# Kernel tuning notes

Measured on AMD Instinct MI355X. Metric: run time of the kernel, lower is better.

The kernel has to match this reference:

```python
import jax, jax.numpy as jnp
import numpy as np

N_TOK = 16384   # total tokens (batch*seq)
H = 2048        # hidden_size
I = 768         # moe_intermediate_size (per-expert MLP width)
TOPK = 8        # num_experts_per_tok


def setup_inputs() -> dict:
    key = jax.random.key(0)
    ks = jax.random.split(key, 7)
    hidden_states = jax.random.normal(ks[0], (N_TOK, H), dtype=jnp.float32)
    # expert_mask[j, k] != 0 means token k selected this expert at top-k slot j
    expert_mask = jax.random.randint(ks[1], (TOPK, N_TOK), 0, 2, dtype=jnp.int32)
    routing_weights = jax.random.uniform(ks[2], (N_TOK, TOPK), dtype=jnp.float32)
    final_hidden_states = jax.random.normal(ks[3], (N_TOK, H), dtype=jnp.float32)
    gate_w = jax.random.normal(ks[4], (I, H), dtype=jnp.float32) * 0.02
    up_w = jax.random.normal(ks[5], (I, H), dtype=jnp.float32) * 0.02
    down_w = jax.random.normal(ks[6], (H, I), dtype=jnp.float32) * 0.02
    return {
        "hidden_states": hidden_states,
        "expert_mask": expert_mask,
        "routing_weights": routing_weights,
        "final_hidden_states": final_hidden_states,
        "gate_w": gate_w,
        "up_w": up_w,
        "down_w": down_w,
    }


def reference(hidden_states, expert_mask, routing_weights, final_hidden_states,
              gate_w, up_w, down_w):
    # forward_expert: gather selected tokens, SwiGLU MLP, scale by routing weight,
    # scatter-add into final_hidden_states. Equivalent jit-friendly form: the
    # combined routing weight per token is w[k] = sum_j mask[j,k]*routing_weights[k,j]
    # (tokens selected multiple times are summed, matching index_add_ semantics),
    # and unselected tokens get w[k]=0 so they contribute nothing.
    g = hidden_states @ gate_w.T                       # [N, I]
    u = hidden_states @ up_w.T                         # [N, I]
    y = (jax.nn.silu(g) * u) @ down_w.T                # [N, H]
    w = jnp.einsum('jk,kj->k', expert_mask.astype(y.dtype), routing_weights)  # [N]
    return final_hidden_states + y * w[:, None]
```

## Files before the change

### kernel.cpp

```cpp
#include <hip/hip_runtime.h>
#include <stdint.h>

#define NTOK 16384
#define HD   2048
#define ID   768
#define TOPK 8

typedef __bf16 bf16x8 __attribute__((ext_vector_type(8)));
typedef float  floatx4 __attribute__((ext_vector_type(4)));
typedef unsigned short ushort8 __attribute__((ext_vector_type(8)));

__device__ __forceinline__ unsigned short f32_to_bf16_rne(float f) {
    union { float f; uint32_t u; } v; v.f = f;
    uint32_t u = v.u;
    u += 0x7FFFu + ((u >> 16) & 1u);
    return (unsigned short)(u >> 16);
}
__device__ __forceinline__ float bf16_to_f32(unsigned short h) {
    union { uint32_t u; float f; } v; v.u = ((uint32_t)h) << 16;
    return v.f;
}

#define GLD_LDS(gsrc, ldst)                                                              \
    __builtin_amdgcn_global_load_lds(                                                    \
        (const __attribute__((address_space(1))) uint32_t*)(const void*)(gsrc),          \
        (__attribute__((address_space(3))) uint32_t*)(void*)(ldst), 16, 0, 0)

template<int VM> __device__ __forceinline__ void wait_vm() {
    if constexpr (VM == 8)      asm volatile("s_waitcnt vmcnt(8)" ::: "memory");
    else if constexpr (VM == 4) asm volatile("s_waitcnt vmcnt(4)" ::: "memory");
    else if constexpr (VM == 3) asm volatile("s_waitcnt vmcnt(3)" ::: "memory");
    else                        asm volatile("s_waitcnt vmcnt(0)" ::: "memory");
}
#define BARRIER() do { asm volatile("" ::: "memory");              \
                       __builtin_amdgcn_s_barrier();               \
                       asm volatile("" ::: "memory"); } while (0)

__global__ __launch_bounds__(256) void compute_w_kernel(const int* __restrict__ mask,
                                                        const float* __restrict__ rw,
                                                        float* __restrict__ w) {
    int k = blockIdx.x * 256 + threadIdx.x;
    if (k >= NTOK) return;
    float acc = 0.f;
#pragma unroll
    for (int j = 0; j < TOPK; ++j)
        acc += (float)mask[j * NTOK + k] * rw[k * TOPK + j];
    w[k] = acc;
}

__global__ __launch_bounds__(256) void convert_hs_kernel(const float* __restrict__ src,
                                                         unsigned short* __restrict__ dst) {
    size_t i = (size_t)blockIdx.x * 256 + threadIdx.x;
    const float4* s = (const float4*)src;
    float4 a = s[2 * i], b = s[2 * i + 1];
    ushort8 o;
    o[0] = f32_to_bf16_rne(a.x); o[1] = f32_to_bf16_rne(a.y);
    o[2] = f32_to_bf16_rne(a.z); o[3] = f32_to_bf16_rne(a.w);
    o[4] = f32_to_bf16_rne(b.x); o[5] = f32_to_bf16_rne(b.y);
    o[6] = f32_to_bf16_rne(b.z); o[7] = f32_to_bf16_rne(b.w);
    *(ushort8*)(dst + 8 * i) = o;
}

__global__ __launch_bounds__(256) void convert_w3_kernel(const float* __restrict__ g,
                                                         const float* __restrict__ u,
                                                         const float* __restrict__ d,
                                                         unsigned short* __restrict__ dst) {
    int i = blockIdx.x * 256 + threadIdx.x;
    size_t e = (size_t)i * 8;
    const float* src;
    if (e < (size_t)2 * ID * HD) {
        int rd = (int)(e / HD);
        int c  = (int)(e - (size_t)rd * HD);
        int b = rd >> 4, h = (rd >> 3) & 1, sub = rd & 7;
        src = (h ? u : g) + (size_t)(b * 8 + sub) * HD + c;
    } else {
        src = d + (e - (size_t)2 * ID * HD);
    }
    const float4* s = (const float4*)src;
    float4 a = s[0], bq = s[1];
    ushort8 o;
    o[0] = f32_to_bf16_rne(a.x);  o[1] = f32_to_bf16_rne(a.y);
    o[2] = f32_to_bf16_rne(a.z);  o[3] = f32_to_bf16_rne(a.w);
    o[4] = f32_to_bf16_rne(bq.x); o[5] = f32_to_bf16_rne(bq.y);
    o[6] = f32_to_bf16_rne(bq.z); o[7] = f32_to_bf16_rne(bq.w);
    *(ushort8*)(dst + e) = o;
}

__global__ __launch_bounds__(512, 1) void gemm_gu_kernel(
    const unsigned short* __restrict__ A,
    const unsigned short* __restrict__ B,
    unsigned short* __restrict__ act) {
    constexpr int K = HD;
    constexpr int NT = K / 64;
    __shared__ __align__(16) unsigned char lds[2][57344];

    const int bid = blockIdx.x, nwg = gridDim.x;
    const int nb = (bid & 7) * (nwg >> 3) + (bid >> 3);
    const int bx = nb & 7, by = nb >> 3;
    const int row0 = by * 256, col0 = bx * 192;

    const int tid = threadIdx.x, wid = tid >> 6, lane = tid & 63;
    const int wr = wid >> 2, wc = wid & 3;
    const int lrow = lane & 15, q = lane >> 4;
    const int rsw = ((q ^ ((lrow >> 1) & 3)) << 4);

    const int kswz = (((lane & 3) ^ ((lane >> 3) & 3)) << 3);
    const unsigned short* sA[2];
#pragma unroll
    for (int h = 0; h < 2; ++h) {
        const int o = h * 8192 + wid * 1024 + lane * 16;
        sA[h] = A + (size_t)(row0 + (o >> 6)) * K + kswz;
    }
    const unsigned short* sB[3];
#pragma unroll
    for (int r = 0; r < 3; ++r) {
        const int o = r * 8192 + tid * 16;
        const int ks = (o >= 12288) ? 1 : 0;
        const int brow = (o - ks * 12288) >> 6;
        sB[r] = B + (size_t)(col0 + brow) * K + ks * 32 + kswz;
    }

#define STAGE_A(sb, ks, kt) do {                                                            \
        GLD_LDS(sA[0] + (kt) * 64 + (ks) * 32, lds[sb] + (ks) * 16384 + wid * 1024);        \
        GLD_LDS(sA[1] + (kt) * 64 + (ks) * 32, lds[sb] + (ks) * 16384 + 8192 + wid * 1024); \
    } while (0)
#define STAGE_B01(sb, kt) do {                                                              \
        GLD_LDS(sB[0] + (kt) * 64, lds[sb] + 32768 + wid * 1024);                           \
        GLD_LDS(sB[1] + (kt) * 64, lds[sb] + 32768 + 8192 + wid * 1024);                    \
    } while (0)
#define STAGE_B2(sb, kt)                                                                    \
        GLD_LDS(sB[2] + (kt) * 64, lds[sb] + 32768 + 16384 + wid * 1024)

#define READ_A(s, ks) do { const unsigned char* rgn = lds[s] + (ks) * 16384;                \
        _Pragma("unroll")                                                                   \
        for (int m = 0; m < 8; ++m)                                                         \
            af[m] = *(const bf16x8*)(rgn + (wr * 128 + m * 16 + lrow) * 64 + rsw);          \
    } while (0)
#define READ_B(s, ks) do { const unsigned char* rgn = lds[s] + 32768 + (ks) * 12288;        \
        _Pragma("unroll")                                                                   \
        for (int n = 0; n < 3; ++n)                                                         \
            bb[n] = *(const bf16x8*)(rgn + (wc * 48 + n * 16 + lrow) * 64 + rsw);           \
    } while (0)
#define MFMA_H(mh) do {                                                                     \
        __builtin_amdgcn_s_setprio(1);                                                      \
        _Pragma("unroll")                                                                   \
        for (int m = (mh) * 4; m < (mh) * 4 + 4; ++m)                                       \
            _Pragma("unroll")                                                               \
            for (int n = 0; n < 3; ++n)                                                     \
                acc[m][n] = __builtin_amdgcn_mfma_f32_16x16x32_bf16(af[m], bb[n], acc[m][n], 0, 0, 0); \
        __builtin_amdgcn_s_setprio(0);                                                      \
    } while (0)

    floatx4 acc[8][3];
#pragma unroll
    for (int m = 0; m < 8; ++m)
#pragma unroll
        for (int n = 0; n < 3; ++n) acc[m][n] = (floatx4){0.f, 0.f, 0.f, 0.f};
    bf16x8 af[8], bb[3];

    STAGE_A(0, 0, 0);
    STAGE_B01(0, 0);
    STAGE_A(0, 1, 0);
    STAGE_B2(0, 0);
    wait_vm<3>();
    BARRIER();

    for (int t = 0; t < NT - 1; ++t) {
        const int s = t & 1, sn = s ^ 1;
        READ_A(s, 0); READ_B(s, 0);
        STAGE_A(sn, 0, t + 1);
        MFMA_H(0);
        BARRIER();
        STAGE_B01(sn, t + 1);
        MFMA_H(1);
        wait_vm<4>();
        BARRIER();
        READ_A(s, 1); READ_B(s, 1);
        STAGE_A(sn, 1, t + 1);
        MFMA_H(0);
        BARRIER();
        STAGE_B2(sn, t + 1);
        MFMA_H(1);
        wait_vm<3>();
        BARRIER();
    }
    {
        const int s = (NT - 1) & 1;
        READ_A(s, 0); READ_B(s, 0);
        MFMA_H(0);
        BARRIER();
        MFMA_H(1);
        wait_vm<0>();
        BARRIER();
        READ_A(s, 1); READ_B(s, 1);
        MFMA_H(0);
        MFMA_H(1);
    }
#undef STAGE_A
#undef STAGE_B01
#undef STAGE_B2
#undef READ_A
#undef READ_B
#undef MFMA_H

#pragma unroll
    for (int m = 0; m < 8; ++m) {
        const int rowb = row0 + wr * 128 + m * 16 + q * 4;
        float sv[3][4];
#pragma unroll
        for (int n = 0; n < 3; ++n)
#pragma unroll
            for (int r = 0; r < 4; ++r) {
                const float gf = acc[m][n][r];
                const float uf = __shfl_xor(gf, 8, 64);
                const float sig = __builtin_amdgcn_rcpf(1.f + __expf(-gf));
                sv[n][r] = gf * sig * uf;
            }
        if ((lrow & 8) == 0) {
            const int ib0 = (col0 >> 1) + wc * 24 + lrow;
#pragma unroll
            for (int n = 0; n < 3; ++n)
#pragma unroll
                for (int r = 0; r < 4; ++r)
                    act[(size_t)(rowb + r) * ID + ib0 + n * 8] = f32_to_bf16_rne(sv[n][r]);
        }
    }
}

__global__ __launch_bounds__(256, 2) void gemm_down_kernel(
    const unsigned short* __restrict__ A,
    const unsigned short* __restrict__ B,
    const float* __restrict__ fin,
    const float* __restrict__ wtok,
    float* __restrict__ out) {
    constexpr int K = ID;
    constexpr int NT = K / 64;
    __shared__ __align__(16) unsigned char lds[2][32768];

    const int bid = blockIdx.x, nwg = gridDim.x;
    const int nb = (bid & 7) * (nwg >> 3) + (bid >> 3);
    const int bx = nb & 15, by = nb >> 4;
    const int row0 = by * 128, col0 = bx * 128;

    const int tid = threadIdx.x, wid = tid >> 6, lane = tid & 63;
    const int wr = wid >> 1, wc = wid & 1;
    const int lrow = lane & 15, q = lane >> 4;

    const int srow = wid * 8 + (lane >> 3);
    const int sk = (((lane & 7) ^ ((lane >> 3) & 7)) << 3);
    const unsigned short* sA[4];
    const unsigned short* sB[4];
#pragma unroll
    for (int r = 0; r < 4; ++r) {
        sA[r] = A + (size_t)(row0 + r * 32 + srow) * K + sk;
        sB[r] = B + (size_t)(col0 + r * 32 + srow) * K + sk;
    }

#define STAGE_T(sb, kt) do {                                                    \
        _Pragma("unroll")                                                       \
        for (int r = 0; r < 4; ++r)                                             \
            GLD_LDS(sA[r] + (kt) * 64, lds[sb] + r * 4096 + wid * 1024);        \
        _Pragma("unroll")                                                       \
        for (int r = 0; r < 4; ++r)                                             \
            GLD_LDS(sB[r] + (kt) * 64, lds[sb] + 16384 + r * 4096 + wid * 1024);\
    } while (0)

    floatx4 acc[4][4];
#pragma unroll
    for (int m = 0; m < 4; ++m)
#pragma unroll
        for (int n = 0; n < 4; ++n) acc[m][n] = (floatx4){0.f, 0.f, 0.f, 0.f};
    bf16x8 af[4], bb[4];

    STAGE_T(0, 0);

    for (int t = 0; t < NT; ++t) {
        const int s = t & 1;
        if (t + 1 < NT) {
            STAGE_T(s ^ 1, t + 1);
            wait_vm<8>();
        } else {
            wait_vm<0>();
        }
        BARRIER();
        const unsigned char* la = lds[s];
        const unsigned char* lb = lds[s] + 16384;
#pragma unroll
        for (int ks = 0; ks < 2; ++ks) {
#pragma unroll
            for (int m = 0; m < 4; ++m)
                af[m] = *(const bf16x8*)(la + (wr * 64 + m * 16 + lrow) * 128 +
                                         (((ks * 4 + q) ^ (lrow & 7)) << 4));
#pragma unroll
            for (int n = 0; n < 4; ++n)
                bb[n] = *(const bf16x8*)(lb + (wc * 64 + n * 16 + lrow) * 128 +
                                         (((ks * 4 + q) ^ (lrow & 7)) << 4));
            __builtin_amdgcn_s_setprio(1);
#pragma unroll
            for (int m = 0; m < 4; ++m)
#pragma unroll
                for (int n = 0; n < 4; ++n)
                    acc[m][n] = __builtin_amdgcn_mfma_f32_16x16x32_bf16(af[m], bb[n], acc[m][n], 0, 0, 0);
            __builtin_amdgcn_s_setprio(0);
        }
        BARRIER();
    }
#undef STAGE_T

#pragma unroll
    for (int m = 0; m < 4; ++m)
#pragma unroll
        for (int r = 0; r < 4; ++r) {
            const int row = row0 + wr * 64 + m * 16 + q * 4 + r;
            const float wv = wtok[row];
#pragma unroll
            for (int n = 0; n < 4; ++n) {
                const int col = col0 + wc * 64 + n * 16 + lrow;
                out[(size_t)row * HD + col] = fin[(size_t)row * HD + col] + wv * acc[m][n][r];
            }
        }
}

extern "C" void kernel_launch(void* const* d_in, const int* in_sizes, int n_in,
                              void* d_out, int out_size, void* d_ws, size_t ws_size,
                              hipStream_t stream) {
    const float* hs   = (const float*)d_in[0];
    const int*   mask = (const int*)d_in[1];
    const float* rw   = (const float*)d_in[2];
    const float* fin  = (const float*)d_in[3];
    const float* gw   = (const float*)d_in[4];
    const float* uw   = (const float*)d_in[5];
    const float* dw   = (const float*)d_in[6];
    float* out = (float*)d_out;

    char* ws = (char*)d_ws;
    unsigned short* hs_b   = (unsigned short*)ws; ws += (size_t)NTOK * HD * 2;
    unsigned short* wcat_b = (unsigned short*)ws; ws += (size_t)3 * ID * HD * 2;
    unsigned short* act_b  = (unsigned short*)ws; ws += (size_t)NTOK * ID * 2;
    float* wtok = (float*)ws;
    unsigned short* down_b = wcat_b + (size_t)2 * ID * HD;

    compute_w_kernel<<<NTOK / 256, 256, 0, stream>>>(mask, rw, wtok);
    convert_hs_kernel<<<(NTOK * HD / 8) / 256, 256, 0, stream>>>(hs, hs_b);
    convert_w3_kernel<<<(3 * ID * HD / 8) / 256, 256, 0, stream>>>(gw, uw, dw, wcat_b);

    gemm_gu_kernel<<<512, 512, 0, stream>>>(hs_b, wcat_b, act_b);

    gemm_down_kernel<<<2048, 256, 0, stream>>>(act_b, down_b, fin, wtok, out);
}
```

Measured before the change: 224.6 us.

## Software-pipeline LDS fragment reads behind MFMA in gate/up GEMM main loop

Splits the A/B LDS fragment loads into half-tiles and issues each next half's ds_reads right after the current half's MFMAs, with double-buffered register fragments. Global-to-LDS staging and vmcnt waits are re-placed, and the next k-tile's first fragments are preloaded at the end of each iteration. The goal is to hide LDS read latency behind matrix math instead of stalling before each MFMA group. In exchange it uses more VGPRs for the extra fragment buffers, which could lower occupancy or cause spills. The changed barrier and wait placement also risks LDS read/write hazards.

Result: no change. 224.9 us (+0.1%).

```diff
diff --git a/kernel.cpp b/kernel.cpp
--- a/kernel.cpp
+++ b/kernel.cpp
@@ -28,8 +28,8 @@
 
 template<int VM> __device__ __forceinline__ void wait_vm() {
     if constexpr (VM == 8)      asm volatile("s_waitcnt vmcnt(8)" ::: "memory");
-    else if constexpr (VM == 4) asm volatile("s_waitcnt vmcnt(4)" ::: "memory");
     else if constexpr (VM == 3) asm volatile("s_waitcnt vmcnt(3)" ::: "memory");
+    else if constexpr (VM == 2) asm volatile("s_waitcnt vmcnt(2)" ::: "memory");
     else                        asm volatile("s_waitcnt vmcnt(0)" ::: "memory");
 }
 #define BARRIER() do { asm volatile("" ::: "memory");              \
@@ -131,23 +131,23 @@
 #define STAGE_B2(sb, kt)                                                                    \
         GLD_LDS(sB[2] + (kt) * 64, lds[sb] + 32768 + 16384 + wid * 1024)
 
-#define READ_A(s, ks) do { const unsigned char* rgn = lds[s] + (ks) * 16384;                \
+#define READ_A4(dstv, sb, ks, mh) do { const unsigned char* rgn = lds[sb] + (ks) * 16384;   \
         _Pragma("unroll")                                                                   \
-        for (int m = 0; m < 8; ++m)                                                         \
-            af[m] = *(const bf16x8*)(rgn + (wr * 128 + m * 16 + lrow) * 64 + rsw);          \
-    } while (0)
-#define READ_B(s, ks) do { const unsigned char* rgn = lds[s] + 32768 + (ks) * 12288;        \
+        for (int m = 0; m < 4; ++m)                                                         \
+            dstv[m] = *(const bf16x8*)(rgn + (wr * 128 + ((mh) * 4 + m) * 16 + lrow) * 64 + rsw); \
+    } while (0)
+#define READ_B3(dstv, sb, ks) do { const unsigned char* rgn = lds[sb] + 32768 + (ks) * 12288; \
         _Pragma("unroll")                                                                   \
         for (int n = 0; n < 3; ++n)                                                         \
-            bb[n] = *(const bf16x8*)(rgn + (wc * 48 + n * 16 + lrow) * 64 + rsw);           \
-    } while (0)
-#define MFMA_H(mh) do {                                                                     \
+            dstv[n] = *(const bf16x8*)(rgn + (wc * 48 + n * 16 + lrow) * 64 + rsw);         \
+    } while (0)
+#define MFMA12(av, bv, mh) do {                                                             \
         __builtin_amdgcn_s_setprio(1);                                                      \
         _Pragma("unroll")                                                                   \
-        for (int m = (mh) * 4; m < (mh) * 4 + 4; ++m)                                       \
+        for (int m = 0; m < 4; ++m)                                                         \
             _Pragma("unroll")                                                               \
             for (int n = 0; n < 3; ++n)                                                     \
-                acc[m][n] = __builtin_amdgcn_mfma_f32_16x16x32_bf16(af[m], bb[n], acc[m][n], 0, 0, 0); \
+                acc[(mh) * 4 + m][n] = __builtin_amdgcn_mfma_f32_16x16x32_bf16(av[m], bv[n], acc[(mh) * 4 + m][n], 0, 0, 0); \
         __builtin_amdgcn_s_setprio(0);                                                      \
     } while (0)
 
@@ -156,7 +156,7 @@
     for (int m = 0; m < 8; ++m)
 #pragma unroll
         for (int n = 0; n < 3; ++n) acc[m][n] = (floatx4){0.f, 0.f, 0.f, 0.f};
-    bf16x8 af[8], bb[3];
+    bf16x8 a03[4], a47[4], a03n[4], a47n[4], bb0[3], bb1[3];
 
     STAGE_A(0, 0, 0);
     STAGE_B01(0, 0);
@@ -164,44 +164,52 @@
     STAGE_B2(0, 0);
     wait_vm<3>();
     BARRIER();
+    READ_A4(a03, 0, 0, 0);
+    READ_B3(bb0, 0, 0);
 
     for (int t = 0; t < NT - 1; ++t) {
         const int s = t & 1, sn = s ^ 1;
-        READ_A(s, 0); READ_B(s, 0);
         STAGE_A(sn, 0, t + 1);
-        MFMA_H(0);
+        MFMA12(a03, bb0, 0);
+        READ_A4(a47, s, 0, 1);
+        wait_vm<2>();
         BARRIER();
         STAGE_B01(sn, t + 1);
-        MFMA_H(1);
-        wait_vm<4>();
-        BARRIER();
-        READ_A(s, 1); READ_B(s, 1);
+        MFMA12(a47, bb0, 1);
+        READ_A4(a03n, s, 1, 0);
+        READ_B3(bb1, s, 1);
+        BARRIER();
         STAGE_A(sn, 1, t + 1);
-        MFMA_H(0);
-        BARRIER();
         STAGE_B2(sn, t + 1);
-        MFMA_H(1);
+        MFMA12(a03n, bb1, 0);
+        READ_A4(a47n, s, 1, 1);
         wait_vm<3>();
+        BARRIER();
+        MFMA12(a47n, bb1, 1);
+        READ_A4(a03, sn, 0, 0);
+        READ_B3(bb0, sn, 0);
         BARRIER();
     }
     {
         const int s = (NT - 1) & 1;
-        READ_A(s, 0); READ_B(s, 0);
-        MFMA_H(0);
-        BARRIER();
-        MFMA_H(1);
+        MFMA12(a03, bb0, 0);
+        READ_A4(a47, s, 0, 1);
         wait_vm<0>();
         BARRIER();
-        READ_A(s, 1); READ_B(s, 1);
-        MFMA_H(0);
-        MFMA_H(1);
+        MFMA12(a47, bb0, 1);
+        READ_A4(a03n, s, 1, 0);
+        READ_B3(bb1, s, 1);
+        BARRIER();
+        MFMA12(a03n, bb1, 0);
+        READ_A4(a47n, s, 1, 1);
+        MFMA12(a47n, bb1, 1);
     }
 #undef STAGE_A
 #undef STAGE_B01
 #undef STAGE_B2
-#undef READ_A
-#undef READ_B
-#undef MFMA_H
+#undef READ_A4
+#undef READ_B3
+#undef MFMA12
 
 #pragma unroll
     for (int m = 0; m < 8; ++m) {
```
